# Kernel optimization log

Hardware: AMD Instinct MI355X
Metric: run time of the kernel (lower is better)

The kernel has to match this reference:

```python
import jax, jax.numpy as jnp
import numpy as np

H = 128  # hidden width of the PINN MLP


def _mlp_scalar(pt, W0, b0, W1, b1, W2, b2, W3, b3):
    # pt: [2] -> scalar u(x, y); tanh MLP as used in PINN solid-mechanics nets
    h = jnp.tanh(pt @ W0 + b0)
    h = jnp.tanh(h @ W1 + b1)
    h = jnp.tanh(h @ W2 + b2)
    return (h @ W3 + b3)[0]


def setup_inputs() -> dict:
    key = jax.random.key(0)
    ks = jax.random.split(key, 6)
    N = 131072
    # Xavier-ish scaling so tanh stays in its smooth regime
    X = jax.random.normal(ks[0], (N, 2), dtype=jnp.float32)
    W0 = jax.random.normal(ks[1], (2, H), dtype=jnp.float32) * (1.0 / np.sqrt(2.0))
    b0 = jnp.zeros((H,), dtype=jnp.float32)
    W1 = jax.random.normal(ks[2], (H, H), dtype=jnp.float32) * (1.0 / np.sqrt(H))
    b1 = jnp.zeros((H,), dtype=jnp.float32)
    W2 = jax.random.normal(ks[3], (H, H), dtype=jnp.float32) * (1.0 / np.sqrt(H))
    b2 = jnp.zeros((H,), dtype=jnp.float32)
    W3 = jax.random.normal(ks[4], (H, 1), dtype=jnp.float32) * (1.0 / np.sqrt(H))
    b3 = jnp.zeros((1,), dtype=jnp.float32)
    return {"X": X, "W0": W0, "b0": b0, "W1": W1, "b1": b1,
            "W2": W2, "b2": b2, "W3": W3, "b3": b3}


def reference(X, W0, b0, W1, b1, W2, b2, W3, b3):
    # Per-point Hessian of u w.r.t. (x, y). Each collocation point is
    # independent, so TF's batched gradient-of-sum equals the per-point
    # derivative; forward-over-reverse (jacfwd o jacrev) vmapped over N is
    # the efficient fused form of the two nested GradientTapes.
    f = lambda pt: _mlp_scalar(pt, W0, b0, W1, b1, W2, b2, W3, b3)
    hess = jax.vmap(jax.jacfwd(jax.jacrev(f)))(X)  # [N, 2, 2]
    du_dxx = hess[:, 0, 0][:, None]  # [N, 1]
    du_dxy = hess[:, 0, 1][:, None]  # [N, 1]
    du_dyy = hess[:, 1, 1][:, None]  # [N, 1]
    return (du_dxx, du_dxy, du_dyy)
```

## Files before the change

kernel.cpp:

```cpp
#include <hip/hip_runtime.h>

#define H   128
#define P   16
#define NT  512

typedef _Float16 v8h __attribute__((ext_vector_type(8)));
typedef __fp16   h2  __attribute__((ext_vector_type(2)));
typedef float    v4f __attribute__((ext_vector_type(4)));
typedef float    v2f __attribute__((ext_vector_type(2)));

union PK2 { h2 h[2]; uint2 u; };

__device__ __forceinline__ int soct(int pl, int p, int o) {
    return ((pl * P + p) * 16 + (o ^ (p & 15))) << 3;
}

__global__ void wt_convert(const float* __restrict__ W1,
                           const float* __restrict__ W2,
                           _Float16* __restrict__ ws) {
    const int t = blockIdx.x * 64 + threadIdx.x;
    const int l = t >> 13;
    const int r = t & 8191;
    const int oct = r >> 9;
    const int rem = r & 511;
    const int j  = rem >> 2;
    const int wp = rem & 3;
    const int k  = oct * 8 + 2 * wp;
    const float* __restrict__ W = l ? W2 : W1;
    const float a = W[k * H + j];
    const float b = W[(k + 1) * H + j];
    union { h2 h; unsigned u; } q;
    q.h = __builtin_amdgcn_cvt_pkrtz(a, b);
    ((unsigned*)ws)[t] = q.u;
}

__device__ __forceinline__ v2f tanh_d2_p(v2f z, v2f& g1, v2f& g2) {
    v2f r;
    r.x = __builtin_amdgcn_rcpf(__expf(2.f * z.x) + 1.f);
    r.y = __builtin_amdgcn_rcpf(__expf(2.f * z.y) + 1.f);
    const v2f a = -2.f * r + 1.f;
    g1 = 1.f - a * a;
    g2 = -2.f * (a * g1);
    return a;
}

__global__ __launch_bounds__(NT, 8)
void pinn_hess_mfma(const float* __restrict__ X,
                    const float* __restrict__ W0, const float* __restrict__ b0,
                    const _Float16* __restrict__ Wt,
                    const float* __restrict__ b1, const float* __restrict__ b2,
                    const float* __restrict__ W3,
                    float* __restrict__ out, int N)
{
    __shared__ _Float16 sS[6 * P * H];

    const int tid   = threadIdx.x;
    const int jquad = tid >> 6;
    const int lane  = tid & 63;
    const int quad  = lane >> 4;
    const int l15   = lane & 15;
    const int pbase = blockIdx.x * P;
    const int pmy   = l15;

    {
        const int p = tid >> 5, q4 = tid & 31;
        const float x = X[2 * (pbase + p)];
        const float y = X[2 * (pbase + p) + 1];
        const float4 wx4 = *(const float4*)&W0[q4 * 4];
        const float4 wy4 = *(const float4*)&W0[H + q4 * 4];
        const float4 bb4 = *(const float4*)&b0[q4 * 4];
        PK2 q[6];
        #pragma unroll
        for (int hp = 0; hp < 2; ++hp) {
            const v2f wx = hp ? (v2f){wx4.z, wx4.w} : (v2f){wx4.x, wx4.y};
            const v2f wy = hp ? (v2f){wy4.z, wy4.w} : (v2f){wy4.x, wy4.y};
            const v2f bb = hp ? (v2f){bb4.z, bb4.w} : (v2f){bb4.x, bb4.y};
            v2f g1, g2;
            const v2f a = tanh_d2_p(x * wx + y * wy + bb, g1, g2);
            const v2f gx = g2 * wx;
            const v2f r0 = a,        r1 = g1 * wx,  r2 = g1 * wy;
            const v2f r3 = gx * wx,  r4 = gx * wy,  r5 = (g2 * wy) * wy;
            q[0].h[hp] = __builtin_amdgcn_cvt_pkrtz(r0.x, r0.y);
            q[1].h[hp] = __builtin_amdgcn_cvt_pkrtz(r1.x, r1.y);
            q[2].h[hp] = __builtin_amdgcn_cvt_pkrtz(r2.x, r2.y);
            q[3].h[hp] = __builtin_amdgcn_cvt_pkrtz(r3.x, r3.y);
            q[4].h[hp] = __builtin_amdgcn_cvt_pkrtz(r4.x, r4.y);
            q[5].h[hp] = __builtin_amdgcn_cvt_pkrtz(r5.x, r5.y);
        }
        const int o  = q4 >> 1;
        const int ho = (q4 & 1) * 4;
        #pragma unroll
        for (int pl = 0; pl < 6; ++pl)
            *(uint2*)&sS[soct(pl, p, o) + ho] = q[pl].u;
    }

    const int aoff = quad * H + jquad * 16 + l15;

    for (int layer = 0; layer < 2; ++layer) {
        const v8h* __restrict__ Ag = (const v8h*)(Wt + layer * (16 * H * 8));

        __syncthreads();

        v4f C[6];
        #pragma unroll
        for (int pl = 0; pl < 6; ++pl) C[pl] = (v4f){0, 0, 0, 0};

        #pragma unroll
        for (int kc = 0; kc < 4; ++kc) {
            const v8h A = Ag[aoff + kc * 4 * H];
            const int oct = kc * 4 + quad;
            #pragma unroll
            for (int pl = 0; pl < 6; ++pl) {
                const v8h B = *(const v8h*)&sS[soct(pl, pmy, oct)];
                C[pl] = __builtin_amdgcn_mfma_f32_16x16x32_f16(A, B, C[pl], 0, 0, 0);
            }
        }

        __syncthreads();

        const int j0 = jquad * 16 + quad * 4;

        if (layer == 0) {
            const float4 bv = *(const float4*)&b1[j0];
            PK2 q[6];
            #pragma unroll
            for (int hp = 0; hp < 2; ++hp) {
                const v2f zb = hp ? (v2f){C[0][2], C[0][3]} : (v2f){C[0][0], C[0][1]};
                const v2f bb = hp ? (v2f){bv.z, bv.w}       : (v2f){bv.x, bv.y};
                const v2f tx = hp ? (v2f){C[1][2], C[1][3]} : (v2f){C[1][0], C[1][1]};
                const v2f ty = hp ? (v2f){C[2][2], C[2][3]} : (v2f){C[2][0], C[2][1]};
                const v2f cx = hp ? (v2f){C[3][2], C[3][3]} : (v2f){C[3][0], C[3][1]};
                const v2f cm = hp ? (v2f){C[4][2], C[4][3]} : (v2f){C[4][0], C[4][1]};
                const v2f cy = hp ? (v2f){C[5][2], C[5][3]} : (v2f){C[5][0], C[5][1]};
                v2f g1, g2;
                const v2f a  = tanh_d2_p(zb + bb, g1, g2);
                const v2f gx = g2 * tx;
                const v2f s0 = a,        s1 = g1 * tx,          s2 = g1 * ty;
                const v2f s3 = gx * tx + g1 * cx;
                const v2f s4 = gx * ty + g1 * cm;
                const v2f s5 = (g2 * ty) * ty + g1 * cy;
                q[0].h[hp] = __builtin_amdgcn_cvt_pkrtz(s0.x, s0.y);
                q[1].h[hp] = __builtin_amdgcn_cvt_pkrtz(s1.x, s1.y);
                q[2].h[hp] = __builtin_amdgcn_cvt_pkrtz(s2.x, s2.y);
                q[3].h[hp] = __builtin_amdgcn_cvt_pkrtz(s3.x, s3.y);
                q[4].h[hp] = __builtin_amdgcn_cvt_pkrtz(s4.x, s4.y);
                q[5].h[hp] = __builtin_amdgcn_cvt_pkrtz(s5.x, s5.y);
            }
            const int ob = j0 >> 3;
            const int ho = (quad & 1) * 4;
            #pragma unroll
            for (int pl = 0; pl < 6; ++pl)
                *(uint2*)&sS[soct(pl, pmy, ob) + ho] = q[pl].u;
        } else {
            v2f axx = {0.f, 0.f}, axy = {0.f, 0.f}, ayy = {0.f, 0.f};
            const float4 bv = *(const float4*)&b2[j0];
            const float4 wv = *(const float4*)&W3[j0];
            #pragma unroll
            for (int hp = 0; hp < 2; ++hp) {
                const v2f zb = hp ? (v2f){C[0][2], C[0][3]} : (v2f){C[0][0], C[0][1]};
                const v2f bb = hp ? (v2f){bv.z, bv.w}       : (v2f){bv.x, bv.y};
                const v2f w3 = hp ? (v2f){wv.z, wv.w}       : (v2f){wv.x, wv.y};
                const v2f tx = hp ? (v2f){C[1][2], C[1][3]} : (v2f){C[1][0], C[1][1]};
                const v2f ty = hp ? (v2f){C[2][2], C[2][3]} : (v2f){C[2][0], C[2][1]};
                const v2f cx = hp ? (v2f){C[3][2], C[3][3]} : (v2f){C[3][0], C[3][1]};
                const v2f cm = hp ? (v2f){C[4][2], C[4][3]} : (v2f){C[4][0], C[4][1]};
                const v2f cy = hp ? (v2f){C[5][2], C[5][3]} : (v2f){C[5][0], C[5][1]};
                v2f g1, g2;
                tanh_d2_p(zb + bb, g1, g2);
                const v2f gx = g2 * tx;
                axx = axx + w3 * (gx * tx + g1 * cx);
                axy = axy + w3 * (gx * ty + g1 * cm);
                ayy = ayy + w3 * ((g2 * ty) * ty + g1 * cy);
            }
            float oxx = axx.x + axx.y, oxy = axy.x + axy.y, oyy = ayy.x + ayy.y;
            oxx += __shfl_xor(oxx, 16); oxx += __shfl_xor(oxx, 32);
            oxy += __shfl_xor(oxy, 16); oxy += __shfl_xor(oxy, 32);
            oyy += __shfl_xor(oyy, 16); oyy += __shfl_xor(oyy, 32);
            float* sRed = (float*)sS;
            if (quad == 0) {
                sRed[0 * 128 + jquad * 16 + pmy] = oxx;
                sRed[1 * 128 + jquad * 16 + pmy] = oxy;
                sRed[2 * 128 + jquad * 16 + pmy] = oyy;
            }
            __syncthreads();
            if (tid < 48) {
                const int c = tid >> 4, p = tid & 15;
                float acc = 0.f;
                #pragma unroll
                for (int jq = 0; jq < 8; ++jq)
                    acc += sRed[c * 128 + jq * 16 + p];
                out[c * N + pbase + p] = acc;
            }
        }
    }
}

extern "C" void kernel_launch(void* const* d_in, const int* in_sizes, int n_in,
                              void* d_out, int out_size, void* d_ws, size_t ws_size,
                              hipStream_t stream) {
    const float* X  = (const float*)d_in[0];
    const float* W0 = (const float*)d_in[1];
    const float* b0 = (const float*)d_in[2];
    const float* W1 = (const float*)d_in[3];
    const float* b1 = (const float*)d_in[4];
    const float* W2 = (const float*)d_in[5];
    const float* b2 = (const float*)d_in[6];
    const float* W3 = (const float*)d_in[7];

    const int N = in_sizes[0] / 2;
    float* out = (float*)d_out;
    _Float16* ws = (_Float16*)d_ws;

    hipLaunchKernelGGL(wt_convert, dim3(256), dim3(64), 0, stream, W1, W2, ws);

    hipLaunchKernelGGL(pinn_hess_mfma, dim3(N / P), dim3(NT), 0, stream,
                       X, W0, b0, ws, b1, b2, W3, out, N);
}
```

Measured before the change: 136.6 us.

## Split waves into plane groups with 32-wide output tiles and share primal/tangent via LDS

Work is redistributed across the 8 waves: each wave now covers 32 output columns (two 16-row A tiles reused against each B load) and only 3 of the 6 jet planes, instead of 16 columns times all 6 planes. The value and first-derivative accumulators of wave group 0 are staged through a new fp32 shared buffer so group 1 can compute second-derivative terms. The aim is to halve B-fragment LDS reads per MFMA and cut accumulator registers, at the cost of an extra LDS round trip, an extra barrier per layer, and a final layer where only half the waves do epilogue work.

```diff
diff --git a/kernel.cpp b/kernel.cpp
--- a/kernel.cpp
+++ b/kernel.cpp
@@ -13,6 +13,10 @@
 
 __device__ __forceinline__ int soct(int pl, int p, int o) {
     return ((pl * P + p) * 16 + (o ^ (p & 15))) << 3;
+}
+
+__device__ __forceinline__ int axi(int jw, int pp, int pt, int jb) {
+    return ((jw * 3 + pp) * 16 + pt) * 32 + (jb ^ ((pt & 7) << 2));
 }
 
 __global__ void wt_convert(const float* __restrict__ W1,
@@ -53,9 +57,12 @@
                     float* __restrict__ out, int N)
 {
     __shared__ _Float16 sS[6 * P * H];
+    __shared__ float    sAux[4 * 3 * P * 32];
 
     const int tid   = threadIdx.x;
-    const int jquad = tid >> 6;
+    const int wave  = tid >> 6;
+    const int plg   = wave >> 2;
+    const int jw    = wave & 3;
     const int lane  = tid & 63;
     const int quad  = lane >> 4;
     const int l15   = lane & 15;
@@ -94,101 +101,168 @@
             *(uint2*)&sS[soct(pl, p, o) + ho] = q[pl].u;
     }
 
-    const int aoff = quad * H + jquad * 16 + l15;
-
+    const int aoff = quad * H + jw * 32 + l15;
+
+    #pragma unroll
     for (int layer = 0; layer < 2; ++layer) {
         const v8h* __restrict__ Ag = (const v8h*)(Wt + layer * (16 * H * 8));
 
         __syncthreads();
-
-        v4f C[6];
-        #pragma unroll
-        for (int pl = 0; pl < 6; ++pl) C[pl] = (v4f){0, 0, 0, 0};
+        __builtin_amdgcn_sched_barrier(0);
+
+        v4f C[2][3];
+        #pragma unroll
+        for (int mt = 0; mt < 2; ++mt)
+            #pragma unroll
+            for (int pp = 0; pp < 3; ++pp) C[mt][pp] = (v4f){0, 0, 0, 0};
 
         #pragma unroll
         for (int kc = 0; kc < 4; ++kc) {
-            const v8h A = Ag[aoff + kc * 4 * H];
+            const v8h A0 = Ag[aoff + kc * 4 * H];
+            const v8h A1 = Ag[aoff + kc * 4 * H + 16];
             const int oct = kc * 4 + quad;
             #pragma unroll
-            for (int pl = 0; pl < 6; ++pl) {
-                const v8h B = *(const v8h*)&sS[soct(pl, pmy, oct)];
-                C[pl] = __builtin_amdgcn_mfma_f32_16x16x32_f16(A, B, C[pl], 0, 0, 0);
-            }
+            for (int pp = 0; pp < 3; ++pp) {
+                const v8h B = *(const v8h*)&sS[soct(plg * 3 + pp, pmy, oct)];
+                C[0][pp] = __builtin_amdgcn_mfma_f32_16x16x32_f16(A0, B, C[0][pp], 0, 0, 0);
+                C[1][pp] = __builtin_amdgcn_mfma_f32_16x16x32_f16(A1, B, C[1][pp], 0, 0, 0);
+            }
+            __builtin_amdgcn_sched_barrier(0);
         }
 
         __syncthreads();
 
-        const int j0 = jquad * 16 + quad * 4;
+        if (plg == 0) {
+            #pragma unroll
+            for (int mt = 0; mt < 2; ++mt) {
+                const int jb = mt * 16 + quad * 4;
+                #pragma unroll
+                for (int pp = 0; pp < 3; ++pp)
+                    *(v4f*)&sAux[axi(jw, pp, l15, jb)] = C[mt][pp];
+            }
+        }
+        __syncthreads();
 
         if (layer == 0) {
-            const float4 bv = *(const float4*)&b1[j0];
-            PK2 q[6];
-            #pragma unroll
-            for (int hp = 0; hp < 2; ++hp) {
-                const v2f zb = hp ? (v2f){C[0][2], C[0][3]} : (v2f){C[0][0], C[0][1]};
-                const v2f bb = hp ? (v2f){bv.z, bv.w}       : (v2f){bv.x, bv.y};
-                const v2f tx = hp ? (v2f){C[1][2], C[1][3]} : (v2f){C[1][0], C[1][1]};
-                const v2f ty = hp ? (v2f){C[2][2], C[2][3]} : (v2f){C[2][0], C[2][1]};
-                const v2f cx = hp ? (v2f){C[3][2], C[3][3]} : (v2f){C[3][0], C[3][1]};
-                const v2f cm = hp ? (v2f){C[4][2], C[4][3]} : (v2f){C[4][0], C[4][1]};
-                const v2f cy = hp ? (v2f){C[5][2], C[5][3]} : (v2f){C[5][0], C[5][1]};
-                v2f g1, g2;
-                const v2f a  = tanh_d2_p(zb + bb, g1, g2);
-                const v2f gx = g2 * tx;
-                const v2f s0 = a,        s1 = g1 * tx,          s2 = g1 * ty;
-                const v2f s3 = gx * tx + g1 * cx;
-                const v2f s4 = gx * ty + g1 * cm;
-                const v2f s5 = (g2 * ty) * ty + g1 * cy;
-                q[0].h[hp] = __builtin_amdgcn_cvt_pkrtz(s0.x, s0.y);
-                q[1].h[hp] = __builtin_amdgcn_cvt_pkrtz(s1.x, s1.y);
-                q[2].h[hp] = __builtin_amdgcn_cvt_pkrtz(s2.x, s2.y);
-                q[3].h[hp] = __builtin_amdgcn_cvt_pkrtz(s3.x, s3.y);
-                q[4].h[hp] = __builtin_amdgcn_cvt_pkrtz(s4.x, s4.y);
-                q[5].h[hp] = __builtin_amdgcn_cvt_pkrtz(s5.x, s5.y);
-            }
-            const int ob = j0 >> 3;
-            const int ho = (quad & 1) * 4;
-            #pragma unroll
-            for (int pl = 0; pl < 6; ++pl)
-                *(uint2*)&sS[soct(pl, pmy, ob) + ho] = q[pl].u;
+            if (plg == 0) {
+                #pragma unroll
+                for (int mt = 0; mt < 2; ++mt) {
+                    const int j0 = jw * 32 + mt * 16 + quad * 4;
+                    const float4 bv = *(const float4*)&b1[j0];
+                    PK2 q[3];
+                    #pragma unroll
+                    for (int hp = 0; hp < 2; ++hp) {
+                        const v2f zb = hp ? (v2f){C[mt][0][2], C[mt][0][3]}
+                                          : (v2f){C[mt][0][0], C[mt][0][1]};
+                        const v2f bb = hp ? (v2f){bv.z, bv.w} : (v2f){bv.x, bv.y};
+                        const v2f tx = hp ? (v2f){C[mt][1][2], C[mt][1][3]}
+                                          : (v2f){C[mt][1][0], C[mt][1][1]};
+                        const v2f ty = hp ? (v2f){C[mt][2][2], C[mt][2][3]}
+                                          : (v2f){C[mt][2][0], C[mt][2][1]};
+                        v2f g1, g2;
+                        const v2f a  = tanh_d2_p(zb + bb, g1, g2);
+                        const v2f s1 = g1 * tx, s2 = g1 * ty;
+                        q[0].h[hp] = __builtin_amdgcn_cvt_pkrtz(a.x,  a.y);
+                        q[1].h[hp] = __builtin_amdgcn_cvt_pkrtz(s1.x, s1.y);
+                        q[2].h[hp] = __builtin_amdgcn_cvt_pkrtz(s2.x, s2.y);
+                    }
+                    const int ob = j0 >> 3;
+                    const int ho = (quad & 1) * 4;
+                    #pragma unroll
+                    for (int pl = 0; pl < 3; ++pl)
+                        *(uint2*)&sS[soct(pl, pmy, ob) + ho] = q[pl].u;
+                }
+            } else {
+                #pragma unroll
+                for (int mt = 0; mt < 2; ++mt) {
+                    const int jb = mt * 16 + quad * 4;
+                    const int j0 = jw * 32 + jb;
+                    const v4f zv  = *(const v4f*)&sAux[axi(jw, 0, l15, jb)];
+                    const v4f txv = *(const v4f*)&sAux[axi(jw, 1, l15, jb)];
+                    const v4f tyv = *(const v4f*)&sAux[axi(jw, 2, l15, jb)];
+                    const float4 bv = *(const float4*)&b1[j0];
+                    PK2 q[3];
+                    #pragma unroll
+                    for (int hp = 0; hp < 2; ++hp) {
+                        const v2f zb = hp ? (v2f){zv[2], zv[3]}   : (v2f){zv[0], zv[1]};
+                        const v2f bb = hp ? (v2f){bv.z, bv.w}     : (v2f){bv.x, bv.y};
+                        const v2f tx = hp ? (v2f){txv[2], txv[3]} : (v2f){txv[0], txv[1]};
+                        const v2f ty = hp ? (v2f){tyv[2], tyv[3]} : (v2f){tyv[0], tyv[1]};
+                        const v2f cx = hp ? (v2f){C[mt][0][2], C[mt][0][3]}
+                                          : (v2f){C[mt][0][0], C[mt][0][1]};
+                        const v2f cm = hp ? (v2f){C[mt][1][2], C[mt][1][3]}
+                                          : (v2f){C[mt][1][0], C[mt][1][1]};
+                        const v2f cy = hp ? (v2f){C[mt][2][2], C[mt][2][3]}
+                                          : (v2f){C[mt][2][0], C[mt][2][1]};
+                        v2f g1, g2;
+                        tanh_d2_p(zb + bb, g1, g2);
+                        const v2f gx = g2 * tx;
+                        const v2f s3 = gx * tx + g1 * cx;
+                        const v2f s4 = gx * ty + g1 * cm;
+                        const v2f s5 = (g2 * ty) * ty + g1 * cy;
+                        q[0].h[hp] = __builtin_amdgcn_cvt_pkrtz(s3.x, s3.y);
+                        q[1].h[hp] = __builtin_amdgcn_cvt_pkrtz(s4.x, s4.y);
+                        q[2].h[hp] = __builtin_amdgcn_cvt_pkrtz(s5.x, s5.y);
+                    }
+                    const int ob = j0 >> 3;
+                    const int ho = (quad & 1) * 4;
+                    #pragma unroll
+                    for (int pl = 0; pl < 3; ++pl)
+                        *(uint2*)&sS[soct(3 + pl, pmy, ob) + ho] = q[pl].u;
+                }
+            }
         } else {
-            v2f axx = {0.f, 0.f}, axy = {0.f, 0.f}, ayy = {0.f, 0.f};
-            const float4 bv = *(const float4*)&b2[j0];
-            const float4 wv = *(const float4*)&W3[j0];
-            #pragma unroll
-            for (int hp = 0; hp < 2; ++hp) {
-                const v2f zb = hp ? (v2f){C[0][2], C[0][3]} : (v2f){C[0][0], C[0][1]};
-                const v2f bb = hp ? (v2f){bv.z, bv.w}       : (v2f){bv.x, bv.y};
-                const v2f w3 = hp ? (v2f){wv.z, wv.w}       : (v2f){wv.x, wv.y};
-                const v2f tx = hp ? (v2f){C[1][2], C[1][3]} : (v2f){C[1][0], C[1][1]};
-                const v2f ty = hp ? (v2f){C[2][2], C[2][3]} : (v2f){C[2][0], C[2][1]};
-                const v2f cx = hp ? (v2f){C[3][2], C[3][3]} : (v2f){C[3][0], C[3][1]};
-                const v2f cm = hp ? (v2f){C[4][2], C[4][3]} : (v2f){C[4][0], C[4][1]};
-                const v2f cy = hp ? (v2f){C[5][2], C[5][3]} : (v2f){C[5][0], C[5][1]};
-                v2f g1, g2;
-                tanh_d2_p(zb + bb, g1, g2);
-                const v2f gx = g2 * tx;
-                axx = axx + w3 * (gx * tx + g1 * cx);
-                axy = axy + w3 * (gx * ty + g1 * cm);
-                ayy = ayy + w3 * ((g2 * ty) * ty + g1 * cy);
-            }
-            float oxx = axx.x + axx.y, oxy = axy.x + axy.y, oyy = ayy.x + ayy.y;
-            oxx += __shfl_xor(oxx, 16); oxx += __shfl_xor(oxx, 32);
-            oxy += __shfl_xor(oxy, 16); oxy += __shfl_xor(oxy, 32);
-            oyy += __shfl_xor(oyy, 16); oyy += __shfl_xor(oyy, 32);
-            float* sRed = (float*)sS;
-            if (quad == 0) {
-                sRed[0 * 128 + jquad * 16 + pmy] = oxx;
-                sRed[1 * 128 + jquad * 16 + pmy] = oxy;
-                sRed[2 * 128 + jquad * 16 + pmy] = oyy;
+            if (plg == 1) {
+                v2f axx = {0.f, 0.f}, axy = {0.f, 0.f}, ayy = {0.f, 0.f};
+                #pragma unroll
+                for (int mt = 0; mt < 2; ++mt) {
+                    const int jb = mt * 16 + quad * 4;
+                    const int j0 = jw * 32 + jb;
+                    const v4f zv  = *(const v4f*)&sAux[axi(jw, 0, l15, jb)];
+                    const v4f txv = *(const v4f*)&sAux[axi(jw, 1, l15, jb)];
+                    const v4f tyv = *(const v4f*)&sAux[axi(jw, 2, l15, jb)];
+                    const float4 bv = *(const float4*)&b2[j0];
+                    const float4 wv = *(const float4*)&W3[j0];
+                    #pragma unroll
+                    for (int hp = 0; hp < 2; ++hp) {
+                        const v2f zb = hp ? (v2f){zv[2], zv[3]}   : (v2f){zv[0], zv[1]};
+                        const v2f bb = hp ? (v2f){bv.z, bv.w}     : (v2f){bv.x, bv.y};
+                        const v2f w3 = hp ? (v2f){wv.z, wv.w}     : (v2f){wv.x, wv.y};
+                        const v2f tx = hp ? (v2f){txv[2], txv[3]} : (v2f){txv[0], txv[1]};
+                        const v2f ty = hp ? (v2f){tyv[2], tyv[3]} : (v2f){tyv[0], tyv[1]};
+                        const v2f cx = hp ? (v2f){C[mt][0][2], C[mt][0][3]}
+                                          : (v2f){C[mt][0][0], C[mt][0][1]};
+                        const v2f cm = hp ? (v2f){C[mt][1][2], C[mt][1][3]}
+                                          : (v2f){C[mt][1][0], C[mt][1][1]};
+                        const v2f cy = hp ? (v2f){C[mt][2][2], C[mt][2][3]}
+                                          : (v2f){C[mt][2][0], C[mt][2][1]};
+                        v2f g1, g2;
+                        tanh_d2_p(zb + bb, g1, g2);
+                        const v2f gx = g2 * tx;
+                        axx = axx + w3 * (gx * tx + g1 * cx);
+                        axy = axy + w3 * (gx * ty + g1 * cm);
+                        ayy = ayy + w3 * ((g2 * ty) * ty + g1 * cy);
+                    }
+                }
+                float oxx = axx.x + axx.y, oxy = axy.x + axy.y, oyy = ayy.x + ayy.y;
+                oxx += __shfl_xor(oxx, 16); oxx += __shfl_xor(oxx, 32);
+                oxy += __shfl_xor(oxy, 16); oxy += __shfl_xor(oxy, 32);
+                oyy += __shfl_xor(oyy, 16); oyy += __shfl_xor(oyy, 32);
+                float* sRed = (float*)sS;
+                if (quad == 0) {
+                    sRed[0 * 64 + jw * 16 + pmy] = oxx;
+                    sRed[1 * 64 + jw * 16 + pmy] = oxy;
+                    sRed[2 * 64 + jw * 16 + pmy] = oyy;
+                }
             }
             __syncthreads();
             if (tid < 48) {
+                float* sRed = (float*)sS;
                 const int c = tid >> 4, p = tid & 15;
                 float acc = 0.f;
                 #pragma unroll
-                for (int jq = 0; jq < 8; ++jq)
-                    acc += sRed[c * 128 + jq * 16 + p];
+                for (int jq = 0; jq < 4; ++jq)
+                    acc += sRed[c * 64 + jq * 16 + p];
                 out[c * N + pbase + p] = acc;
             }
         }
```

Measured after the change: 151.6 us. 11.0% more time.
